# Performance work log

Measured on AMD Instinct MI355X. Metric: run time of the kernel, lower is better.

## Reference

```python
import math
import jax, jax.numpy as jnp
import numpy as np

C = 1024
H = 16
HD = C // H
T = 2048
B = 2
EPS = 1e-5


def setup_inputs() -> dict:
    key = jax.random.key(0)
    ks = jax.random.split(key, 8)
    s = 0.02
    return {
        "x": jax.random.normal(ks[0], (B, T, C), dtype=jnp.float32),
        "ln1_g": jnp.ones((C,), jnp.float32),
        "ln1_b": jnp.zeros((C,), jnp.float32),
        "w_attn": jax.random.normal(ks[1], (C, 3 * C), dtype=jnp.float32) * s,
        "b_attn": jnp.zeros((3 * C,), jnp.float32),
        "w_proj": jax.random.normal(ks[2], (C, C), dtype=jnp.float32) * s,
        "b_proj": jnp.zeros((C,), jnp.float32),
        "ln2_g": jnp.ones((C,), jnp.float32),
        "ln2_b": jnp.zeros((C,), jnp.float32),
        "w_fc": jax.random.normal(ks[3], (C, 4 * C), dtype=jnp.float32) * s,
        "b_fc": jnp.zeros((4 * C,), jnp.float32),
        "w_fc2": jax.random.normal(ks[4], (4 * C, C), dtype=jnp.float32) * s,
        "b_fc2": jnp.zeros((C,), jnp.float32),
    }


def _layernorm(x, g, b):
    mu = jnp.mean(x, axis=-1, keepdims=True)
    var = jnp.mean((x - mu) ** 2, axis=-1, keepdims=True)
    return (x - mu) * jax.lax.rsqrt(var + EPS) * g + b


def _attention(x, w_attn, b_attn, w_proj, b_proj):
    Bb, Tt, Cc = x.shape
    qkv = x @ w_attn + b_attn  # (B,T,3C)
    q, k, v = jnp.split(qkv, 3, axis=-1)
    # (B,H,T,HD)
    q = q.reshape(Bb, Tt, H, HD).transpose(0, 2, 1, 3)
    k = k.reshape(Bb, Tt, H, HD).transpose(0, 2, 1, 3)
    v = v.reshape(Bb, Tt, H, HD).transpose(0, 2, 1, 3)
    scale = 1.0 / math.sqrt(HD)
    attn = jnp.einsum("bhqd,bhkd->bhqk", q, k) * scale
    causal = jnp.tril(jnp.ones((Tt, Tt), dtype=bool))
    attn = jnp.where(causal[None, None], attn, -jnp.inf)
    attn = jax.nn.softmax(attn, axis=-1)
    out = jnp.einsum("bhqk,bhkd->bhqd", attn, v)
    out = out.transpose(0, 2, 1, 3).reshape(Bb, Tt, Cc)
    return out @ w_proj + b_proj


def _mlp(x, w_fc, b_fc, w_fc2, b_fc2):
    h = jax.nn.gelu(x @ w_fc + b_fc, approximate=True)
    return h @ w_fc2 + b_fc2


def reference(x, ln1_g, ln1_b, w_attn, b_attn, w_proj, b_proj,
              ln2_g, ln2_b, w_fc, b_fc, w_fc2, b_fc2):
    x = x + _attention(_layernorm(x, ln1_g, ln1_b), w_attn, b_attn, w_proj, b_proj)
    x = x + _mlp(_layernorm(x, ln2_g, ln2_b), w_fc, b_fc, w_fc2, b_fc2)
    return x
```

## Files before the change

kernel.cpp:

```cpp
#include <hip/hip_runtime.h>
#include <math.h>

#define TB 2
#define TT 2048
#define TC 1024
#define TH 16
#define THD 64
#define TM (TB*TT)
#define NQT 32

typedef __bf16 bf16x8 __attribute__((ext_vector_type(8)));
typedef float f32x4 __attribute__((ext_vector_type(4)));
typedef unsigned short u16x8 __attribute__((ext_vector_type(8)));
typedef unsigned short u16x4 __attribute__((ext_vector_type(4)));

__device__ __forceinline__ unsigned short f2bf(float f){
    unsigned int u = __builtin_bit_cast(unsigned int, f);
    u = (u + 0x7FFFu + ((u >> 16) & 1u)) >> 16;
    return (unsigned short)u;
}
__device__ __forceinline__ float bf2f(unsigned short h){
    unsigned int u = ((unsigned int)h) << 16;
    return __builtin_bit_cast(float, u);
}
__device__ __forceinline__ bf16x8 ldbf8(const unsigned short* p){
    return __builtin_bit_cast(bf16x8, *(const u16x8*)p);
}
__device__ __forceinline__ void gl_lds16(const void* g, void* l){
    __builtin_amdgcn_global_load_lds(
        (const __attribute__((address_space(1))) unsigned int*)g,
        (__attribute__((address_space(3))) unsigned int*)l,
        16, 0, 0);
}
__device__ __forceinline__ float gelu_tanh(float v){
    float u = 2.0f * 0.7978845608028654f * (v + 0.044715f * v * v * v);
    u = fminf(fmaxf(u, -30.f), 30.f);
    float e = __expf(u);
    return 0.5f * v * (1.f + (e - 1.f) / (e + 1.f));
}

__global__ __launch_bounds__(256)
void prep_all(const float* __restrict__ w_attn, const float* __restrict__ w_proj,
              const float* __restrict__ w_fc,   const float* __restrict__ w_fc2,
              unsigned short* __restrict__ wattnT, unsigned short* __restrict__ wprojT,
              unsigned short* __restrict__ wfcT,   unsigned short* __restrict__ wfc2T,
              const float* __restrict__ x, const float* __restrict__ ln1_g,
              const float* __restrict__ ln1_b, unsigned short* __restrict__ xn1){
    const int bid = blockIdx.x;
    const int t = threadIdx.x;
    if (bid >= 12288){
        const int row = bid - 12288;
        const float4* xr = (const float4*)(x + (size_t)row * TC);
        float4 v = xr[t];
        float s  = v.x + v.y + v.z + v.w;
        float s2 = v.x*v.x + v.y*v.y + v.z*v.z + v.w*v.w;
        #pragma unroll
        for (int off = 32; off; off >>= 1){
            s  += __shfl_down(s,  off);
            s2 += __shfl_down(s2, off);
        }
        __shared__ float red[8];
        int l = t & 63, wv = t >> 6;
        if (l == 0){ red[wv] = s; red[4 + wv] = s2; }
        __syncthreads();
        float S  = red[0] + red[1] + red[2] + red[3];
        float S2 = red[4] + red[5] + red[6] + red[7];
        float mu = S * (1.f / TC);
        float var = S2 * (1.f / TC) - mu * mu;
        float rs = rsqrtf(var + 1e-5f);
        int c = t * 4;
        float4 gg = *(const float4*)(ln1_g + c);
        float4 bb = *(const float4*)(ln1_b + c);
        u16x4 o;
        o[0] = f2bf((v.x - mu) * rs * gg.x + bb.x);
        o[1] = f2bf((v.y - mu) * rs * gg.y + bb.y);
        o[2] = f2bf((v.z - mu) * rs * gg.z + bb.z);
        o[3] = f2bf((v.w - mu) * rs * gg.w + bb.w);
        *(u16x4*)(xn1 + (size_t)row * TC + c) = o;
        return;
    }
    __shared__ float tile[32][33];
    const float* in; unsigned short* out; int K, N, bx, by;
    if (bid < 3072)      { in=w_attn; out=wattnT; K=1024; N=3072; bx=bid%96;  by=bid/96; }
    else if (bid < 4096) { int lo=bid-3072; in=w_proj; out=wprojT; K=1024; N=1024; bx=lo%32;  by=lo/32; }
    else if (bid < 8192) { int lo=bid-4096; in=w_fc;   out=wfcT;   K=1024; N=4096; bx=lo%128; by=lo/128; }
    else                 { int lo=bid-8192; in=w_fc2;  out=wfc2T;  K=4096; N=1024; bx=lo%32;  by=lo/32; }
    int tx = t & 31, ty = t >> 5;
    int n0 = bx * 32, k0 = by * 32;
    #pragma unroll
    for (int i = 0; i < 4; i++)
        tile[ty + 8*i][tx] = in[(size_t)(k0 + ty + 8*i) * N + n0 + tx];
    __syncthreads();
    #pragma unroll
    for (int i = 0; i < 4; i++)
        out[(size_t)(n0 + ty + 8*i) * K + k0 + tx] = f2bf(tile[tx][ty + 8*i]);
}

__global__ __launch_bounds__(256)
void ln_kernel(const float* __restrict__ x, const float* __restrict__ g,
               const float* __restrict__ be, unsigned short* __restrict__ y){
    const int row = blockIdx.x, t = threadIdx.x;
    const float4* xr = (const float4*)(x + (size_t)row * TC);
    float4 v = xr[t];
    float s  = v.x + v.y + v.z + v.w;
    float s2 = v.x*v.x + v.y*v.y + v.z*v.z + v.w*v.w;
    #pragma unroll
    for (int off = 32; off; off >>= 1){
        s  += __shfl_down(s,  off);
        s2 += __shfl_down(s2, off);
    }
    __shared__ float red[8];
    int l = t & 63, wv = t >> 6;
    if (l == 0){ red[wv] = s; red[4 + wv] = s2; }
    __syncthreads();
    float S  = red[0] + red[1] + red[2] + red[3];
    float S2 = red[4] + red[5] + red[6] + red[7];
    float mu = S * (1.f / TC);
    float var = S2 * (1.f / TC) - mu * mu;
    float rs = rsqrtf(var + 1e-5f);
    int c = t * 4;
    float4 gg = *(const float4*)(g + c);
    float4 bb = *(const float4*)(be + c);
    u16x4 o;
    o[0] = f2bf((v.x - mu) * rs * gg.x + bb.x);
    o[1] = f2bf((v.y - mu) * rs * gg.y + bb.y);
    o[2] = f2bf((v.z - mu) * rs * gg.z + bb.z);
    o[3] = f2bf((v.w - mu) * rs * gg.w + bb.w);
    *(u16x4*)(y + (size_t)row * TC + c) = o;
}

template<int EPI>
__global__ __launch_bounds__(256, 2)
void gemm_bt(const unsigned short* __restrict__ A,
             const unsigned short* __restrict__ Bt,
             const float* __restrict__ bias,
             const float* __restrict__ resid,
             void* __restrict__ outv,
             int M, int N, int K){
    __shared__ unsigned short lA[128 * 32];
    __shared__ unsigned short lB[128 * 32];
    const int t = threadIdx.x, w = t >> 6, l = t & 63, lr = l & 15, lg = l >> 4;
    const int nt = N >> 7;
    const int nwg = gridDim.x;
    const int bid = blockIdx.x;
    int wg = (nwg & 7) ? bid : ((bid & 7) * (nwg >> 3) + (bid >> 3));
    const int bm = wg / nt, bn = wg % nt;
    const int row0 = bm << 7, col0 = bn << 7;
    const int wr = w >> 1, wc = w & 1;

    f32x4 acc[4][4];
    #pragma unroll
    for (int i = 0; i < 4; i++)
        #pragma unroll
        for (int j = 0; j < 4; j++) acc[i][j] = (f32x4){0.f,0.f,0.f,0.f};

    const char* Ag = (const char*)(A + (size_t)(row0 + (t >> 2)) * K) + (t & 3) * 16;
    const char* Bg = (const char*)(Bt + (size_t)(col0 + (t >> 2)) * K) + (t & 3) * 16;
    const size_t rstep = (size_t)64 * K * 2;
    char* lAw = (char*)lA + w * 1024;
    char* lBw = (char*)lB + w * 1024;

    for (int k0 = 0; k0 < K; k0 += 32){
        size_t kb = (size_t)k0 * 2;
        gl_lds16(Ag + kb,          lAw);
        gl_lds16(Ag + kb + rstep,  lAw + 4096);
        gl_lds16(Bg + kb,          lBw);
        gl_lds16(Bg + kb + rstep,  lBw + 4096);
        __syncthreads();
        bf16x8 af[4], bfr[4];
        #pragma unroll
        for (int mi = 0; mi < 4; mi++)
            af[mi] = ldbf8(lA + (wr*64 + mi*16 + lr) * 32 + lg * 8);
        #pragma unroll
        for (int ni = 0; ni < 4; ni++)
            bfr[ni] = ldbf8(lB + (wc*64 + ni*16 + lr) * 32 + lg * 8);
        #pragma unroll
        for (int mi = 0; mi < 4; mi++)
            #pragma unroll
            for (int ni = 0; ni < 4; ni++)
                acc[mi][ni] = __builtin_amdgcn_mfma_f32_16x16x32_bf16(
                    af[mi], bfr[ni], acc[mi][ni], 0, 0, 0);
        __syncthreads();
    }

    float bcol[4];
    #pragma unroll
    for (int ni = 0; ni < 4; ni++) bcol[ni] = bias[col0 + wc*64 + ni*16 + lr];
    #pragma unroll
    for (int mi = 0; mi < 4; mi++){
        #pragma unroll
        for (int j = 0; j < 4; j++){
            int row = row0 + wr*64 + mi*16 + lg*4 + j;
            size_t base = (size_t)row * N + col0 + wc*64 + lr;
            #pragma unroll
            for (int ni = 0; ni < 4; ni++){
                float v = acc[mi][ni][j] + bcol[ni];
                size_t idx = base + (size_t)ni * 16;
                if (EPI == 0)      ((unsigned short*)outv)[idx] = f2bf(v);
                else if (EPI == 1) ((float*)outv)[idx] = v + resid[idx];
                else               ((unsigned short*)outv)[idx] = f2bf(gelu_tanh(v));
            }
        }
    }
}

template<int MH>
__device__ __forceinline__ void gloadA(const unsigned short* bufA, bf16x8 (&af)[4][2],
                                       int wm, int lr, int sl0, int sl1){
    #pragma unroll
    for (int i = 0; i < 4; i++){
        int lrow = (wm*128 + (MH*4 + i)*16 + lr) * 64;
        af[i][0] = ldbf8(bufA + lrow + sl0);
        af[i][1] = ldbf8(bufA + lrow + sl1);
    }
}
__device__ __forceinline__ void gloadB(const unsigned short* bufB, bf16x8 (&bfr)[4][2],
                                       int wn, int lr, int sl0, int sl1){
    #pragma unroll
    for (int i = 0; i < 4; i++){
        int brow = (wn*64 + i*16 + lr) * 64;
        bfr[i][0] = ldbf8(bufB + brow + sl0);
        bfr[i][1] = ldbf8(bufB + brow + sl1);
    }
}
template<int MH, int NH>
__device__ __forceinline__ void gmma(const bf16x8 (&af)[4][2], const bf16x8 (&bfr)[4][2],
                                     f32x4 (&acc)[8][4]){
    #pragma unroll
    for (int i = 0; i < 4; i++)
        #pragma unroll
        for (int j = 0; j < 2; j++){
            f32x4& a = acc[MH*4 + i][NH*2 + j];
            a = __builtin_amdgcn_mfma_f32_16x16x32_bf16(af[i][0], bfr[NH*2+j][0], a, 0,0,0);
            a = __builtin_amdgcn_mfma_f32_16x16x32_bf16(af[i][1], bfr[NH*2+j][1], a, 0,0,0);
        }
}

#define G256_LOOP(NT_, KBEG_)                                                   \
    for (int tk = 0; tk < (NT_); ++tk){                                         \
        const int cur = tk & 1;                                                 \
        const bool more = (tk + 1) < (NT_);                                     \
        const unsigned short* bufA = &lds[cur][0][0];                           \
        const unsigned short* bufB = &lds[cur][1][0];                           \
        if (more){                                                              \
            stage(cur ^ 1, (KBEG_) + (tk + 1)*64, 0);                           \
            asm volatile("s_waitcnt vmcnt(2)" ::: "memory");                    \
        } else {                                                                \
            asm volatile("s_waitcnt vmcnt(0)" ::: "memory");                    \
        }                                                                       \
        __builtin_amdgcn_s_barrier();                                           \
        bf16x8 af[4][2], bfr[4][2];                                             \
        gloadA<0>(bufA, af, wm, lr, sl0, sl1);                                  \
        gloadB(bufB, bfr, wn, lr, sl0, sl1);                                    \
        if (more) stage(cur ^ 1, (KBEG_) + (tk + 1)*64, 1);                     \
        __builtin_amdgcn_s_barrier();                                           \
        asm volatile("s_waitcnt lgkmcnt(0)" ::: "memory");                      \
        __builtin_amdgcn_sched_barrier(0);                                      \
        __builtin_amdgcn_s_setprio(1);                                          \
        gmma<0,0>(af, bfr, acc);                                                \
        __builtin_amdgcn_s_setprio(0);                                          \
        __builtin_amdgcn_s_barrier();                                           \
        if (more) stage(cur ^ 1, (KBEG_) + (tk + 1)*64, 2);                     \
        __builtin_amdgcn_s_setprio(1);                                          \
        gmma<0,1>(af, bfr, acc);                                                \
        __builtin_amdgcn_s_setprio(0);                                          \
        __builtin_amdgcn_s_barrier();                                           \
        gloadA<1>(bufA, af, wm, lr, sl0, sl1);                                  \
        if (more) stage(cur ^ 1, (KBEG_) + (tk + 1)*64, 3);                     \
        __builtin_amdgcn_s_barrier();                                           \
        asm volatile("s_waitcnt lgkmcnt(0)" ::: "memory");                      \
        __builtin_amdgcn_sched_barrier(0);                                      \
        __builtin_amdgcn_s_setprio(1);                                          \
        gmma<1,0>(af, bfr, acc);                                                \
        __builtin_amdgcn_s_setprio(0);                                          \
        __builtin_amdgcn_s_barrier();                                           \
        __builtin_amdgcn_s_setprio(1);                                          \
        gmma<1,1>(af, bfr, acc);                                                \
        __builtin_amdgcn_s_setprio(0);                                          \
        __builtin_amdgcn_s_barrier();                                           \
    }

template<int EPI>
__global__ __launch_bounds__(512, 1)
void gemm256(const unsigned short* __restrict__ A,
             const unsigned short* __restrict__ Bt,
             const float* __restrict__ bias,
             void* __restrict__ outv,
             int M, int N, int K){
    __shared__ unsigned short lds[2][2][256*64];
    const int t = threadIdx.x;
    const int w = t >> 6, l = t & 63, lr = l & 15, lg = l >> 4;
    const int wm = w >> 2, wn = w & 3;
    const int lr7 = lr & 7;
    const int sl0 = (lg ^ lr7) << 3;
    const int sl1 = ((4 + lg) ^ lr7) << 3;
    const int nbn = N >> 8;
    const int nwg = (M >> 8) * nbn;
    const int bid = blockIdx.x;
    const int wg = (nwg & 7) ? bid : ((bid & 7) * (nwg >> 3) + (bid >> 3));
    const int bm = wg / nbn, bn = wg % nbn;
    const size_t row0 = (size_t)bm << 8, col0 = (size_t)bn << 8;
    const int NT = K >> 6;

    f32x4 acc[8][4];
    #pragma unroll
    for (int i = 0; i < 8; i++)
        #pragma unroll
        for (int j = 0; j < 4; j++) acc[i][j] = (f32x4){0.f,0.f,0.f,0.f};

    int rowc[4], slogc[4];
    #pragma unroll
    for (int c = 0; c < 4; c++){
        int seg = t + (c << 9);
        rowc[c]  = seg >> 3;
        slogc[c] = (((seg & 7) ^ ((seg >> 3) & 7)) << 3);
    }
    const unsigned short* Abase = A  + row0 * K;
    const unsigned short* Bbase = Bt + col0 * K;
    auto stage = [&](int buf, int kofs, int c){
        int seg = t + (c << 9);
        const unsigned short* sa = Abase + (size_t)rowc[c] * K + kofs + slogc[c];
        const unsigned short* sb = Bbase + (size_t)rowc[c] * K + kofs + slogc[c];
        gl_lds16(sa, (void*)&lds[buf][0][seg * 8]);
        gl_lds16(sb, (void*)&lds[buf][1][seg * 8]);
    };

    #pragma unroll
    for (int c = 0; c < 4; c++) stage(0, 0, c);

    G256_LOOP(NT, 0)

    float bcol[4];
    #pragma unroll
    for (int ni = 0; ni < 4; ni++) bcol[ni] = bias[col0 + wn*64 + ni*16 + lr];
    unsigned short* outp = (unsigned short*)outv;
    #pragma unroll
    for (int mi = 0; mi < 8; mi++){
        #pragma unroll
        for (int j = 0; j < 4; j++){
            size_t row = row0 + wm*128 + mi*16 + lg*4 + j;
            size_t base = row * N + col0 + wn*64 + lr;
            #pragma unroll
            for (int ni = 0; ni < 4; ni++){
                float v = acc[mi][ni][j] + bcol[ni];
                size_t idx = base + (size_t)ni * 16;
                if (EPI == 0) outp[idx] = f2bf(v);
                else          outp[idx] = f2bf(gelu_tanh(v));
            }
        }
    }
}

__global__ __launch_bounds__(512, 1)
void gemm256sk(const unsigned short* __restrict__ A,
               const unsigned short* __restrict__ Bt,
               unsigned short* __restrict__ pout,
               int M, int N, int K, int klen){
    __shared__ unsigned short lds[2][2][256*64];
    const int t = threadIdx.x;
    const int w = t >> 6, l = t & 63, lr = l & 15, lg = l >> 4;
    const int wm = w >> 2, wn = w & 3;
    const int lr7 = lr & 7;
    const int sl0 = (lg ^ lr7) << 3;
    const int sl1 = ((4 + lg) ^ lr7) << 3;
    const int nbn = N >> 8;
    const int ntile = (M >> 8) * nbn;
    const int nwg = gridDim.x;
    const int bid = blockIdx.x;
    int wg = (nwg & 7) ? bid : ((bid & 7) * (nwg >> 3) + (bid >> 3));
    const int kh = wg / ntile;
    wg -= kh * ntile;
    const int bm = wg / nbn, bn = wg % nbn;
    const size_t row0 = (size_t)bm << 8, col0 = (size_t)bn << 8;
    const int NT = klen >> 6;
    const int kbeg = kh * klen;

    f32x4 acc[8][4];
    #pragma unroll
    for (int i = 0; i < 8; i++)
        #pragma unroll
        for (int j = 0; j < 4; j++) acc[i][j] = (f32x4){0.f,0.f,0.f,0.f};

    int rowc[4], slogc[4];
    #pragma unroll
    for (int c = 0; c < 4; c++){
        int seg = t + (c << 9);
        rowc[c]  = seg >> 3;
        slogc[c] = (((seg & 7) ^ ((seg >> 3) & 7)) << 3);
    }
    const unsigned short* Abase = A  + row0 * K;
    const unsigned short* Bbase = Bt + col0 * K;
    auto stage = [&](int buf, int kofs, int c){
        int seg = t + (c << 9);
        const unsigned short* sa = Abase + (size_t)rowc[c] * K + kofs + slogc[c];
        const unsigned short* sb = Bbase + (size_t)rowc[c] * K + kofs + slogc[c];
        gl_lds16(sa, (void*)&lds[buf][0][seg * 8]);
        gl_lds16(sb, (void*)&lds[buf][1][seg * 8]);
    };

    #pragma unroll
    for (int c = 0; c < 4; c++) stage(0, kbeg, c);

    G256_LOOP(NT, kbeg)

    unsigned short* outp = pout + (size_t)kh * M * N;
    #pragma unroll
    for (int mi = 0; mi < 8; mi++){
        #pragma unroll
        for (int j = 0; j < 4; j++){
            size_t row = row0 + wm*128 + mi*16 + lg*4 + j;
            size_t base = row * N + col0 + wn*64 + lr;
            #pragma unroll
            for (int ni = 0; ni < 4; ni++)
                outp[base + (size_t)ni * 16] = f2bf(acc[mi][ni][j]);
        }
    }
}

__global__ __launch_bounds__(256)
void combine_k4(const unsigned short* __restrict__ p,
                const float* __restrict__ bias, const float* __restrict__ resid,
                float* __restrict__ out){
    const size_t PS = (size_t)TM * TC;
    const int total = TM * TC / 4;
    for (int i = blockIdx.x * 256 + threadIdx.x; i < total; i += gridDim.x * 256){
        int e = i * 4;
        u16x4 a0 = *(const u16x4*)(p + e);
        u16x4 a1 = *(const u16x4*)(p + PS + e);
        u16x4 a2 = *(const u16x4*)(p + 2*PS + e);
        u16x4 a3 = *(const u16x4*)(p + 3*PS + e);
        float4 r = *(const float4*)(resid + e);
        float4 bb = *(const float4*)(bias + (e & (TC - 1)));
        float4 o;
        o.x = bf2f(a0[0]) + bf2f(a1[0]) + bf2f(a2[0]) + bf2f(a3[0]) + r.x + bb.x;
        o.y = bf2f(a0[1]) + bf2f(a1[1]) + bf2f(a2[1]) + bf2f(a3[1]) + r.y + bb.y;
        o.z = bf2f(a0[2]) + bf2f(a1[2]) + bf2f(a2[2]) + bf2f(a3[2]) + r.z + bb.z;
        o.w = bf2f(a0[3]) + bf2f(a1[3]) + bf2f(a2[3]) + bf2f(a3[3]) + r.w + bb.w;
        *(float4*)(out + e) = o;
    }
}

__global__ __launch_bounds__(256)
void vtrans(const unsigned short* __restrict__ qkv, unsigned short* __restrict__ vTg){
    __shared__ unsigned short lt[64][68];
    int kt = blockIdx.x & (NQT - 1);
    int bh = blockIdx.x >> 5;
    int h = bh & (TH - 1), b = bh >> 4;
    int t = threadIdx.x;
    int r = t >> 2, c4 = t & 3;
    const unsigned short* src = qkv + (size_t)(b*TT + kt*64 + r) * (3*TC) + 2*TC + h*THD;
    u16x8 a0 = *(const u16x8*)(src + c4*8);
    u16x8 a1 = *(const u16x8*)(src + 32 + c4*8);
    #pragma unroll
    for (int j = 0; j < 8; j++){
        lt[r][c4*8 + j]      = a0[j];
        lt[r][32 + c4*8 + j] = a1[j];
    }
    __syncthreads();
    int d = t >> 2;
    unsigned short* dst = vTg + ((size_t)bh * NQT + kt) * (64*80) + (size_t)d * 80;
    u16x8 o0, o1;
    #pragma unroll
    for (int j = 0; j < 8; j++){
        o0[j] = lt[c4*8 + j][d];
        o1[j] = lt[32 + c4*8 + j][d];
    }
    *(u16x8*)(dst + c4*8)      = o0;
    *(u16x8*)(dst + 32 + c4*8) = o1;
}

__global__ __launch_bounds__(256, 4)
void attn_kernel(const unsigned short* __restrict__ qkv,
                 const unsigned short* __restrict__ vTg,
                 unsigned short* __restrict__ attn_out){
    __shared__ unsigned short kbuf[64*64];
    __shared__ unsigned short vbuf[64*64];
    __shared__ unsigned short pl[4][16*72];

    const int bid = blockIdx.x;
    const int qrank = bid >> 5;
    const int bh = bid & 31;
    const int h = bh & (TH - 1), b = bh >> 4;
    const int qb = 31 - qrank;
    const int q0 = qb << 6;
    const int t = threadIdx.x, w = t >> 6, l = t & 63, lr = l & 15, lg = l >> 4;
    const int lr7 = lr & 7;
    const int sl0 = (lg ^ lr7) << 3;
    const int sl1 = ((4 + lg) ^ lr7) << 3;
    const float SC = 0.18033688011112042f;

    const int NKT = qb + 1;
    const int qrow_base = q0 + w*16;

    const int vt0 = t, vt1 = t + 256;
    const int sr0 = vt0 >> 3, sr1 = vt1 >> 3;
    const int sc0 = ((vt0 & 7) ^ (sr0 & 7)) * 8;
    const int sc1 = ((vt1 & 7) ^ (sr1 & 7)) * 8;
    const unsigned short* kg0 = qkv + (size_t)(b*TT + sr0) * (3*TC) + TC + h*THD + sc0;
    const unsigned short* kg1 = qkv + (size_t)(b*TT + sr1) * (3*TC) + TC + h*THD + sc1;
    const unsigned short* vg0 = vTg + (size_t)bh * (NQT*64*80) + (size_t)sr0 * 80 + sc0;
    const unsigned short* vg1 = vTg + (size_t)bh * (NQT*64*80) + (size_t)sr1 * 80 + sc1;
    const size_t kstep = (size_t)64 * (3*TC);

    auto stage = [&](int kt){
        gl_lds16(kg0 + (size_t)kt*kstep,   (void*)&kbuf[vt0*8]);
        gl_lds16(kg1 + (size_t)kt*kstep,   (void*)&kbuf[vt1*8]);
        gl_lds16(vg0 + (size_t)kt*(64*80), (void*)&vbuf[vt0*8]);
        gl_lds16(vg1 + (size_t)kt*(64*80), (void*)&vbuf[vt1*8]);
    };

    const unsigned short* qr =
        qkv + (size_t)(b*TT + qrow_base + lr) * (3*TC) + h*THD;
    bf16x8 q0f = ldbf8(qr + lg*8), q1f = ldbf8(qr + 32 + lg*8);

    bf16x8 ones;
    #pragma unroll
    for (int i = 0; i < 8; i++) ones[i] = (__bf16)1.0f;

    f32x4 o[5];
    float m[4];
    #pragma unroll
    for (int i = 0; i < 5; i++) o[i] = (f32x4){0.f,0.f,0.f,0.f};
    #pragma unroll
    for (int i = 0; i < 4; i++) m[i] = -1e30f;

    unsigned short* plw = &pl[w][0];

    stage(0);
    for (int kt = 0; kt < NKT; ++kt){
        asm volatile("s_waitcnt vmcnt(0)" ::: "memory");
        __builtin_amdgcn_s_barrier();

        f32x4 s[4];
        __builtin_amdgcn_s_setprio(1);
        #pragma unroll
        for (int cb = 0; cb < 4; cb++){
            bf16x8 ka = ldbf8(kbuf + (cb*16 + lr)*64 + sl0);
            bf16x8 kbf = ldbf8(kbuf + (cb*16 + lr)*64 + sl1);
            f32x4 z = (f32x4){0.f,0.f,0.f,0.f};
            z = __builtin_amdgcn_mfma_f32_16x16x32_bf16(q0f, ka, z, 0,0,0);
            z = __builtin_amdgcn_mfma_f32_16x16x32_bf16(q1f, kbf, z, 0,0,0);
            s[cb] = z;
        }
        __builtin_amdgcn_s_setprio(0);
        if (kt == qb){
            #pragma unroll
            for (int cb = 0; cb < 4; cb++)
                #pragma unroll
                for (int j = 0; j < 4; j++)
                    if (kt*64 + cb*16 + lr > qrow_base + lg*4 + j) s[cb][j] = -1e30f;
        }
        float mloc[4];
        #pragma unroll
        for (int j = 0; j < 4; j++)
            mloc[j] = fmaxf(fmaxf(s[0][j], s[1][j]), fmaxf(s[2][j], s[3][j]));
        #pragma unroll
        for (int off = 1; off < 16; off <<= 1)
            #pragma unroll
            for (int j = 0; j < 4; j++)
                mloc[j] = fmaxf(mloc[j], __shfl_xor(mloc[j], off));
        bool grow = (mloc[0]*SC > m[0]) || (mloc[1]*SC > m[1]) ||
                    (mloc[2]*SC > m[2]) || (mloc[3]*SC > m[3]);
        if (__any(grow)){
            float al[4];
            #pragma unroll
            for (int j = 0; j < 4; j++){
                float mn = fmaxf(m[j], mloc[j] * SC);
                al[j] = exp2f(m[j] - mn);
                m[j] = mn;
            }
            #pragma unroll
            for (int db = 0; db < 5; db++)
                #pragma unroll
                for (int j = 0; j < 4; j++) o[db][j] *= al[j];
        }
        #pragma unroll
        for (int cb = 0; cb < 4; cb++)
            #pragma unroll
            for (int j = 0; j < 4; j++){
                float e = exp2f(__builtin_fmaf(s[cb][j], SC, -m[j]));
                ((__bf16*)plw)[(lg*4 + j)*72 + cb*16 + lr] = (__bf16)e;
            }
        bf16x8 pa0 = ldbf8(plw + lr*72 + lg*8);
        bf16x8 pa1 = ldbf8(plw + lr*72 + 32 + lg*8);
        __builtin_amdgcn_s_setprio(1);
        #pragma unroll
        for (int db = 0; db < 4; db++){
            bf16x8 va = ldbf8(vbuf + (db*16 + lr)*64 + sl0);
            bf16x8 vbf = ldbf8(vbuf + (db*16 + lr)*64 + sl1);
            o[db] = __builtin_amdgcn_mfma_f32_16x16x32_bf16(pa0, va, o[db], 0,0,0);
            o[db] = __builtin_amdgcn_mfma_f32_16x16x32_bf16(pa1, vbf, o[db], 0,0,0);
        }
        o[4] = __builtin_amdgcn_mfma_f32_16x16x32_bf16(pa0, ones, o[4], 0,0,0);
        o[4] = __builtin_amdgcn_mfma_f32_16x16x32_bf16(pa1, ones, o[4], 0,0,0);
        __builtin_amdgcn_s_setprio(0);

        __builtin_amdgcn_s_barrier();
        if (kt + 1 < NKT) stage(kt + 1);
    }

    __bf16* aout = (__bf16*)attn_out;
    #pragma unroll
    for (int j = 0; j < 4; j++){
        float inv = 1.f / o[4][j];
        size_t tok = (size_t)(b*TT + qrow_base + lg*4 + j);
        #pragma unroll
        for (int db = 0; db < 4; db++)
            aout[tok*TC + h*THD + db*16 + lr] = (__bf16)(o[db][j] * inv);
    }
}

extern "C" void kernel_launch(void* const* d_in, const int* in_sizes, int n_in,
                              void* d_out, int out_size, void* d_ws, size_t ws_size,
                              hipStream_t stream){
    const float* x      = (const float*)d_in[0];
    const float* ln1_g  = (const float*)d_in[1];
    const float* ln1_b  = (const float*)d_in[2];
    const float* w_attn = (const float*)d_in[3];
    const float* b_attn = (const float*)d_in[4];
    const float* w_proj = (const float*)d_in[5];
    const float* b_proj = (const float*)d_in[6];
    const float* ln2_g  = (const float*)d_in[7];
    const float* ln2_b  = (const float*)d_in[8];
    const float* w_fc   = (const float*)d_in[9];
    const float* b_fc   = (const float*)d_in[10];
    const float* w_fc2  = (const float*)d_in[11];
    const float* b_fc2  = (const float*)d_in[12];
    float* out = (float*)d_out;

    char* ws = (char*)d_ws;
    size_t off = 0;
    auto alloc = [&](size_t bytes) -> void* {
        void* p = ws + off;
        off += (bytes + 255) & ~(size_t)255;
        return p;
    };
    unsigned short* wattnT = (unsigned short*)alloc((size_t)3072*1024*2);
    unsigned short* wprojT = (unsigned short*)alloc((size_t)1024*1024*2);
    unsigned short* wfcT   = (unsigned short*)alloc((size_t)4096*1024*2);
    unsigned short* wfc2T  = (unsigned short*)alloc((size_t)1024*4096*2);
    unsigned short* xn1    = (unsigned short*)alloc((size_t)TM*TC*2);
    unsigned short* qkvb   = (unsigned short*)alloc((size_t)TM*3*TC*2);
    float*          resid1 = (float*)alloc((size_t)TM*TC*4);
    unsigned short* xn2    = (unsigned short*)alloc((size_t)TM*TC*2);
    unsigned short* hbuf   = (unsigned short*)alloc((size_t)TM*4*TC*2);
    unsigned short* attnO  = (unsigned short*)alloc((size_t)TM*TC*2);
    unsigned short* vTg    = (unsigned short*)alloc((size_t)TB*TH*NQT*64*80*2);

    unsigned short* pks = xn1;

    prep_all<<<12288 + TM, 256, 0, stream>>>(
        w_attn, w_proj, w_fc, w_fc2, wattnT, wprojT, wfcT, wfc2T,
        x, ln1_g, ln1_b, xn1);

    gemm256<0><<<(TM/256)*(3072/256), 512, 0, stream>>>(
        xn1, wattnT, b_attn, qkvb, TM, 3072, 1024);

    vtrans<<<TB*TH*NQT, 256, 0, stream>>>(qkvb, vTg);

    attn_kernel<<<TB*TH*NQT, 256, 0, stream>>>(qkvb, vTg, attnO);

    gemm_bt<1><<<(TM/128)*(1024/128), 256, 0, stream>>>(
        attnO, wprojT, b_proj, x, resid1, TM, 1024, 1024);

    ln_kernel<<<TM, 256, 0, stream>>>(resid1, ln2_g, ln2_b, xn2);

    gemm256<2><<<(TM/256)*(4096/256), 512, 0, stream>>>(
        xn2, wfcT, b_fc, hbuf, TM, 4096, 1024);

    gemm256sk<<<4*(TM/256)*(1024/256), 512, 0, stream>>>(
        hbuf, wfc2T, pks, TM, 1024, 4096, 1024);
    combine_k4<<<2048, 256, 0, stream>>>(pks, b_fc2, resid1, out);
}
```

Measured before the change: 235.2 us.

## Process two 64-key tiles per attention loop iteration

The attention kernel now stages and processes 128 keys (two 64-row K/V tiles) per iteration instead of 64. This halves the number of loop iterations, barriers and online-softmax rescales. In exchange, shared memory per block doubles, the occupancy hint drops from 4 to 3 blocks, and query blocks with an even index compute a fully masked extra tile that is thrown away.

```diff
diff --git a/kernel.cpp b/kernel.cpp
--- a/kernel.cpp
+++ b/kernel.cpp
@@ -469,13 +469,13 @@
     *(u16x8*)(dst + 32 + c4*8) = o1;
 }
 
-__global__ __launch_bounds__(256, 4)
+__global__ __launch_bounds__(256, 3)
 void attn_kernel(const unsigned short* __restrict__ qkv,
                  const unsigned short* __restrict__ vTg,
                  unsigned short* __restrict__ attn_out){
-    __shared__ unsigned short kbuf[64*64];
-    __shared__ unsigned short vbuf[64*64];
-    __shared__ unsigned short pl[4][16*72];
+    __shared__ unsigned short kbuf[128*64];
+    __shared__ unsigned short vbuf[128*64];
+    __shared__ unsigned short pl[4][16*136];
 
     const int bid = blockIdx.x;
     const int qrank = bid >> 5;
@@ -489,24 +489,30 @@
     const int sl1 = ((4 + lg) ^ lr7) << 3;
     const float SC = 0.18033688011112042f;
 
-    const int NKT = qb + 1;
+    const int NP = (qb >> 1) + 1;
     const int qrow_base = q0 + w*16;
 
-    const int vt0 = t, vt1 = t + 256;
-    const int sr0 = vt0 >> 3, sr1 = vt1 >> 3;
-    const int sc0 = ((vt0 & 7) ^ (sr0 & 7)) * 8;
-    const int sc1 = ((vt1 & 7) ^ (sr1 & 7)) * 8;
-    const unsigned short* kg0 = qkv + (size_t)(b*TT + sr0) * (3*TC) + TC + h*THD + sc0;
-    const unsigned short* kg1 = qkv + (size_t)(b*TT + sr1) * (3*TC) + TC + h*THD + sc1;
-    const unsigned short* vg0 = vTg + (size_t)bh * (NQT*64*80) + (size_t)sr0 * 80 + sc0;
-    const unsigned short* vg1 = vTg + (size_t)bh * (NQT*64*80) + (size_t)sr1 * 80 + sc1;
-    const size_t kstep = (size_t)64 * (3*TC);
-
-    auto stage = [&](int kt){
-        gl_lds16(kg0 + (size_t)kt*kstep,   (void*)&kbuf[vt0*8]);
-        gl_lds16(kg1 + (size_t)kt*kstep,   (void*)&kbuf[vt1*8]);
-        gl_lds16(vg0 + (size_t)kt*(64*80), (void*)&vbuf[vt0*8]);
-        gl_lds16(vg1 + (size_t)kt*(64*80), (void*)&vbuf[vt1*8]);
+    const unsigned short* kgp[4];
+    const unsigned short* vgp[4];
+    #pragma unroll
+    for (int p = 0; p < 4; p++){
+        int vt = p*256 + t;
+        int r  = vt >> 3;
+        int sc = ((vt & 7) ^ (r & 7)) * 8;
+        kgp[p] = qkv + (size_t)(b*TT + r) * (3*TC) + TC + h*THD + sc;
+        vgp[p] = vTg + (size_t)bh * (NQT*64*80)
+               + (size_t)(r >> 6) * (64*80) + (size_t)(r & 63) * 80 + sc;
+    }
+    const size_t kstep2 = (size_t)128 * (3*TC);
+    const size_t vstep2 = (size_t)2 * (64*80);
+
+    auto stage = [&](int pi){
+        #pragma unroll
+        for (int p = 0; p < 4; p++)
+            gl_lds16(kgp[p] + (size_t)pi*kstep2, (void*)&kbuf[(p*256 + t)*8]);
+        #pragma unroll
+        for (int p = 0; p < 4; p++)
+            gl_lds16(vgp[p] + (size_t)pi*vstep2, (void*)&vbuf[(p*256 + t)*8]);
     };
 
     const unsigned short* qr =
@@ -527,14 +533,15 @@
     unsigned short* plw = &pl[w][0];
 
     stage(0);
-    for (int kt = 0; kt < NKT; ++kt){
+    for (int pi = 0; pi < NP; ++pi){
+        const int t0 = 2*pi, t1 = 2*pi + 1;
         asm volatile("s_waitcnt vmcnt(0)" ::: "memory");
         __builtin_amdgcn_s_barrier();
 
-        f32x4 s[4];
+        f32x4 s[8];
         __builtin_amdgcn_s_setprio(1);
         #pragma unroll
-        for (int cb = 0; cb < 4; cb++){
+        for (int cb = 0; cb < 8; cb++){
             bf16x8 ka = ldbf8(kbuf + (cb*16 + lr)*64 + sl0);
             bf16x8 kbf = ldbf8(kbuf + (cb*16 + lr)*64 + sl1);
             f32x4 z = (f32x4){0.f,0.f,0.f,0.f};
@@ -543,17 +550,32 @@
             s[cb] = z;
         }
         __builtin_amdgcn_s_setprio(0);
-        if (kt == qb){
+        if (t0 == qb){
             #pragma unroll
             for (int cb = 0; cb < 4; cb++)
                 #pragma unroll
                 for (int j = 0; j < 4; j++)
-                    if (kt*64 + cb*16 + lr > qrow_base + lg*4 + j) s[cb][j] = -1e30f;
+                    if (t0*64 + cb*16 + lr > qrow_base + lg*4 + j) s[cb][j] = -1e30f;
+        }
+        if (t1 == qb){
+            #pragma unroll
+            for (int cb = 4; cb < 8; cb++)
+                #pragma unroll
+                for (int j = 0; j < 4; j++)
+                    if (t1*64 + (cb-4)*16 + lr > qrow_base + lg*4 + j) s[cb][j] = -1e30f;
+        } else if (t1 > qb){
+            #pragma unroll
+            for (int cb = 4; cb < 8; cb++)
+                #pragma unroll
+                for (int j = 0; j < 4; j++) s[cb][j] = -1e30f;
         }
         float mloc[4];
         #pragma unroll
-        for (int j = 0; j < 4; j++)
-            mloc[j] = fmaxf(fmaxf(s[0][j], s[1][j]), fmaxf(s[2][j], s[3][j]));
+        for (int j = 0; j < 4; j++){
+            float a = fmaxf(fmaxf(s[0][j], s[1][j]), fmaxf(s[2][j], s[3][j]));
+            float c = fmaxf(fmaxf(s[4][j], s[5][j]), fmaxf(s[6][j], s[7][j]));
+            mloc[j] = fmaxf(a, c);
+        }
         #pragma unroll
         for (int off = 1; off < 16; off <<= 1)
             #pragma unroll
@@ -575,28 +597,36 @@
                 for (int j = 0; j < 4; j++) o[db][j] *= al[j];
         }
         #pragma unroll
-        for (int cb = 0; cb < 4; cb++)
+        for (int cb = 0; cb < 8; cb++)
             #pragma unroll
             for (int j = 0; j < 4; j++){
                 float e = exp2f(__builtin_fmaf(s[cb][j], SC, -m[j]));
-                ((__bf16*)plw)[(lg*4 + j)*72 + cb*16 + lr] = (__bf16)e;
+                ((__bf16*)plw)[(lg*4 + j)*136 + cb*16 + lr] = (__bf16)e;
             }
-        bf16x8 pa0 = ldbf8(plw + lr*72 + lg*8);
-        bf16x8 pa1 = ldbf8(plw + lr*72 + 32 + lg*8);
+        bf16x8 pa0 = ldbf8(plw + lr*136 + lg*8);
+        bf16x8 pa1 = ldbf8(plw + lr*136 + 32 + lg*8);
+        bf16x8 pa2 = ldbf8(plw + lr*136 + 64 + lg*8);
+        bf16x8 pa3 = ldbf8(plw + lr*136 + 96 + lg*8);
         __builtin_amdgcn_s_setprio(1);
         #pragma unroll
         for (int db = 0; db < 4; db++){
-            bf16x8 va = ldbf8(vbuf + (db*16 + lr)*64 + sl0);
-            bf16x8 vbf = ldbf8(vbuf + (db*16 + lr)*64 + sl1);
-            o[db] = __builtin_amdgcn_mfma_f32_16x16x32_bf16(pa0, va, o[db], 0,0,0);
-            o[db] = __builtin_amdgcn_mfma_f32_16x16x32_bf16(pa1, vbf, o[db], 0,0,0);
+            bf16x8 v0a = ldbf8(vbuf + (db*16 + lr)*64 + sl0);
+            bf16x8 v0b = ldbf8(vbuf + (db*16 + lr)*64 + sl1);
+            o[db] = __builtin_amdgcn_mfma_f32_16x16x32_bf16(pa0, v0a, o[db], 0,0,0);
+            o[db] = __builtin_amdgcn_mfma_f32_16x16x32_bf16(pa1, v0b, o[db], 0,0,0);
+            bf16x8 v1a = ldbf8(vbuf + (64 + db*16 + lr)*64 + sl0);
+            bf16x8 v1b = ldbf8(vbuf + (64 + db*16 + lr)*64 + sl1);
+            o[db] = __builtin_amdgcn_mfma_f32_16x16x32_bf16(pa2, v1a, o[db], 0,0,0);
+            o[db] = __builtin_amdgcn_mfma_f32_16x16x32_bf16(pa3, v1b, o[db], 0,0,0);
         }
         o[4] = __builtin_amdgcn_mfma_f32_16x16x32_bf16(pa0, ones, o[4], 0,0,0);
         o[4] = __builtin_amdgcn_mfma_f32_16x16x32_bf16(pa1, ones, o[4], 0,0,0);
+        o[4] = __builtin_amdgcn_mfma_f32_16x16x32_bf16(pa2, ones, o[4], 0,0,0);
+        o[4] = __builtin_amdgcn_mfma_f32_16x16x32_bf16(pa3, ones, o[4], 0,0,0);
         __builtin_amdgcn_s_setprio(0);
 
         __builtin_amdgcn_s_barrier();
-        if (kt + 1 < NKT) stage(kt + 1);
+        if (pi + 1 < NP) stage(pi + 1);
     }
 
     __bf16* aout = (__bf16*)attn_out;
```

Result: faster. 226.2 us (-3.8%).
